# Kernel optimization log

Measured on AMD Instinct MI355X. Metric: run time of the kernel, lower is better.

## Reference

```python
import jax, jax.numpy as jnp
import numpy as np

EPS = 1e-8
TOPK = 12  # hard-coded fallback size in SSP_func


def _cosine(a, b):
    # torch F.cosine_similarity(dim=1): dot / (max(||a||,eps) * max(||b||,eps))
    dot = (a * b).sum(axis=1)
    na = jnp.sqrt((a * a).sum(axis=1))
    nb = jnp.sqrt((b * b).sum(axis=1))
    return dot / (jnp.maximum(na, EPS) * jnp.maximum(nb, EPS))


def _proto(feat, pred_c, thres):
    # feat: (B, C, HW); pred_c: (B, HW) probabilities for one class
    B, C, HW = feat.shape
    mask = pred_c > thres                                   # (B, HW)
    cnt = mask.sum(axis=-1)                                 # (B,)
    masked_mean = (feat * mask[:, None, :].astype(feat.dtype)).sum(-1) / \
        jnp.maximum(cnt, 1).astype(feat.dtype)[:, None]      # (B, C)
    # top-k fallback when no element exceeds threshold
    _, idx = jax.lax.top_k(pred_c, TOPK)                    # (B, TOPK)
    idx_b = jnp.broadcast_to(idx[:, None, :], (B, C, TOPK))
    topk_mean = jnp.take_along_axis(feat, idx_b, axis=-1).mean(-1)  # (B, C)
    return jnp.where((cnt > 0)[:, None], masked_mean, topk_mean)


def _minmax(x):
    return (x - x.min()) / (x.max() - x.min())


def enhence_forward(supp_fp, supp_bp, query_fea, tau):
    B, C, H, W = query_fea.shape
    # similarity_func on support prototypes
    sim_fg = _cosine(query_fea, supp_fp)                    # (B, H, W)
    sim_bg = _cosine(query_fea, supp_bp)
    query_out = jnp.stack([sim_bg, sim_fg], axis=1) * 10.0  # (B, 2, H, W)
    # SSP_func: per-sample threshold mask + topk fallback -> prototypes
    pred = jax.nn.softmax(query_out, axis=1).reshape(B, 2, H * W)
    fg_thres = jax.nn.sigmoid(tau)
    feat = query_fea.reshape(B, C, H * W)
    query_fp = _proto(feat, pred[:, 1], fg_thres)[:, :, None, None]       # (B,C,1,1)
    query_bp = _proto(feat, pred[:, 0], 1.0 - fg_thres)[:, :, None, None]
    # activation maps, global min-max normalized, blend
    act = _minmax(_cosine(query_fea, query_fp)[:, None])    # (B,1,H,W)
    deact = _minmax(_cosine(query_fea, query_bp)[:, None])
    out = query_fea * act + query_fea * (1.0 - deact)
    return out, query_fp, query_bp


def setup_inputs() -> dict:
    key = jax.random.key(0)
    k1, k2, k3 = jax.random.split(key, 3)
    B, C, H, W = 16, 512, 64, 64
    return {
        "supp_fp": jax.random.normal(k1, (B, C, 1, 1), dtype=jnp.float32),
        "supp_bp": jax.random.normal(k2, (B, C, 1, 1), dtype=jnp.float32),
        "query_fea": jax.random.normal(k3, (B, C, H, W), dtype=jnp.float32),
        "tau": jnp.float32(0.5),  # nn.Parameter init value in torch
    }


def reference(supp_fp, supp_bp, query_fea, tau):
    return enhence_forward(supp_fp, supp_bp, query_fea, tau)
```

## Files before the change

### kernel.cpp

```cpp
#include <hip/hip_runtime.h>
#include <math.h>

#define BB 16
#define CC 512
#define HWS 4096
#define EPSV 1e-8f
#define TK 12
#define NEGINF (-3.402823466e+38f)
#define CSPLIT 8
#define CCH (CC / CSPLIT)

typedef float f32x4 __attribute__((ext_vector_type(4)));

#define OFF_PFG 0
#define OFF_PBG (BB * HWS)
#define OFF_QN  (2 * BB * HWS)
#define OFF_CF  (3 * BB * HWS)
#define OFF_CB  (4 * BB * HWS)
#define OFF_SN  (5 * BB * HWS)
#define OFF_PN  (OFF_SN + 2 * BB)
#define OFF_CNT (OFF_PN + 2 * BB)
#define OFF_TKI (OFF_CNT + 2 * BB)
#define OFF_FMMU (OFF_TKI + 2 * BB * TK)
#define OFF_MFG (OFF_FMMU + 16)
#define OFF_MBG (OFF_MFG + BB * 128)
#define OFF_PD1 (OFF_MBG + BB * 128)
#define OFF_PD2 (OFF_PD1 + CSPLIT * BB * HWS)
#define OFF_PQQ (OFF_PD2 + CSPLIT * BB * HWS)

__device__ __forceinline__ float sigmoidf_(float x) { return 1.f / (1.f + expf(-x)); }

__device__ __forceinline__ unsigned encf_(float f) {
    unsigned u = __float_as_uint(f);
    return (u >> 31) ? ~u : (u | 0x80000000u);
}
__device__ __forceinline__ float decf_(unsigned e) {
    return __uint_as_float((e >> 31) ? (e ^ 0x80000000u) : ~e);
}

__global__ void k0_init(const float* __restrict__ sfp, const float* __restrict__ sbp,
                        float* __restrict__ snorm, int* __restrict__ cnts,
                        unsigned* __restrict__ fmmu) {
    if (blockIdx.x == BB) {
        int t = threadIdx.x;
        if (t < 2 * BB) cnts[t] = 0;
        if (t < 4) fmmu[t] = (t & 1) ? 0u : 0xFFFFFFFFu;
        return;
    }
    int b = blockIdx.x;
    int t = threadIdx.x;
    float s1 = 0.f, s2 = 0.f;
    for (int c = t; c < CC; c += 64) {
        float v = sfp[b * CC + c]; s1 += v * v;
        float w = sbp[b * CC + c]; s2 += w * w;
    }
    for (int off = 32; off; off >>= 1) {
        s1 += __shfl_down(s1, off);
        s2 += __shfl_down(s2, off);
    }
    if (t == 0) { snorm[b] = sqrtf(s1); snorm[BB + b] = sqrtf(s2); }
}

__global__ __launch_bounds__(256) void k1_dots(const float* __restrict__ q, const float* __restrict__ sfp,
                        const float* __restrict__ sbp,
                        float* __restrict__ p_df, float* __restrict__ p_db,
                        float* __restrict__ p_qq) {
    int b = blockIdx.z, cs = blockIdx.y;
    int hw4 = blockIdx.x * 256 + threadIdx.x;
    __shared__ float sf[CCH], sb[CCH];
    if (threadIdx.x < CCH) sf[threadIdx.x] = sfp[b * CC + cs * CCH + threadIdx.x];
    else if (threadIdx.x < 2 * CCH) sb[threadIdx.x - CCH] = sbp[b * CC + cs * CCH + (threadIdx.x - CCH)];
    __syncthreads();
    const f32x4* qp4 = (const f32x4*)(q + (size_t)b * CC * HWS + (size_t)cs * CCH * HWS) + hw4;
    f32x4 df = {0, 0, 0, 0}, db = {0, 0, 0, 0}, qq = {0, 0, 0, 0};
#pragma unroll 1
    for (int jj = 0; jj < CCH; jj += 16) {
        f32x4 v[16];
#pragma unroll
        for (int k = 0; k < 16; k++) v[k] = qp4[(size_t)(jj + k) * (HWS / 4)];
#pragma unroll
        for (int k = 0; k < 16; k++) {
            float a = sf[jj + k], c = sb[jj + k];
            df += v[k] * a;
            db += v[k] * c;
            qq += v[k] * v[k];
        }
    }
    size_t o = (size_t)(cs * BB + b) * (HWS / 4) + hw4;
    ((f32x4*)p_df)[o] = df;
    ((f32x4*)p_db)[o] = db;
    ((f32x4*)p_qq)[o] = qq;
}

__global__ __launch_bounds__(256) void k1b_comb(const float* __restrict__ p_df, const float* __restrict__ p_db,
                         const float* __restrict__ p_qq, const float* __restrict__ snorm,
                         const float* __restrict__ tau,
                         float* __restrict__ pfg, float* __restrict__ pbg,
                         float* __restrict__ qn, int* __restrict__ cnts,
                         unsigned* __restrict__ mfg, unsigned* __restrict__ mbg) {
    int b = blockIdx.y;
    int tid = threadIdx.x;
    int hw4 = blockIdx.x * 256 + tid;
    float4 df = {0, 0, 0, 0}, db = {0, 0, 0, 0}, qq = {0, 0, 0, 0};
    for (int cs = 0; cs < CSPLIT; cs++) {
        size_t o = (size_t)(cs * BB + b) * (HWS / 4) + hw4;
        float4 a = ((const float4*)p_df)[o];
        float4 c = ((const float4*)p_db)[o];
        float4 e = ((const float4*)p_qq)[o];
        df.x += a.x; df.y += a.y; df.z += a.z; df.w += a.w;
        db.x += c.x; db.y += c.y; db.z += c.z; db.w += c.w;
        qq.x += e.x; qq.y += e.y; qq.z += e.z; qq.w += e.w;
    }
    float snf = fmaxf(snorm[b], EPSV), snb = fmaxf(snorm[BB + b], EPSV);
    float thres_fg = sigmoidf_(tau[0]);
    float thres_bg = 1.f - thres_fg;
    float dfa[4] = {df.x, df.y, df.z, df.w};
    float dba[4] = {db.x, db.y, db.z, db.w};
    float qqa[4] = {qq.x, qq.y, qq.z, qq.w};
    float pfa[4], pba[4], qna[4];
    unsigned nf = 0, nb = 0;
#pragma unroll
    for (int i = 0; i < 4; i++) {
        float na = sqrtf(qqa[i]);
        float den = fmaxf(na, EPSV);
        float simf = dfa[i] / (den * snf);
        float simb = dba[i] / (den * snb);
        float a = 10.f * simb, c2 = 10.f * simf;
        float m = fmaxf(a, c2);
        float ea = expf(a - m), eb = expf(c2 - m);
        float inv = 1.f / (ea + eb);
        pfa[i] = eb * inv;
        pba[i] = ea * inv;
        qna[i] = na;
        nf |= (pfa[i] > thres_fg ? 1u : 0u) << i;
        nb |= (pba[i] > thres_bg ? 1u : 0u) << i;
    }
    float4 opf = {pfa[0], pfa[1], pfa[2], pfa[3]};
    float4 opb = {pba[0], pba[1], pba[2], pba[3]};
    float4 oqn = {qna[0], qna[1], qna[2], qna[3]};
    size_t o = (size_t)b * (HWS / 4) + hw4;
    ((float4*)pfg)[o] = opf;
    ((float4*)pbg)[o] = opb;
    ((float4*)qn)[o] = oqn;
    __shared__ unsigned char nibf[256], nibb[256];
    nibf[tid] = (unsigned char)nf;
    nibb[tid] = (unsigned char)nb;
    int cfg = __popc(nf), cbg = __popc(nb);
    for (int off = 32; off; off >>= 1) {
        cfg += __shfl_down(cfg, off);
        cbg += __shfl_down(cbg, off);
    }
    if ((tid & 63) == 0) {
        atomicAdd(&cnts[b], cfg);
        atomicAdd(&cnts[BB + b], cbg);
    }
    __syncthreads();
    if (tid < 32) {
        unsigned wf = 0, wb = 0;
#pragma unroll
        for (int k = 0; k < 8; k++) {
            wf |= ((unsigned)nibf[tid * 8 + k]) << (4 * k);
            wb |= ((unsigned)nibb[tid * 8 + k]) << (4 * k);
        }
        mfg[b * 128 + blockIdx.x * 32 + tid] = wf;
        mbg[b * 128 + blockIdx.x * 32 + tid] = wb;
    }
}

__global__ void k2_topk(const float* __restrict__ pfg, const float* __restrict__ pbg,
                        const int* __restrict__ cnts, int* __restrict__ tki) {
    int id = blockIdx.x;
    int cls = id >> 4, b = id & 15;
    if (cnts[cls * BB + b] > 0) return;
    int t = threadIdx.x;
    __shared__ float vals[HWS];
    __shared__ float rv[256];
    __shared__ int   ri[256];
    const float* pr = cls ? pbg : pfg;
    for (int i = t; i < HWS; i += 256) vals[i] = pr[b * HWS + i];
    __syncthreads();
    for (int k = 0; k < TK; k++) {
        float bv = NEGINF; int bi = HWS;
        for (int i = t; i < HWS; i += 256) {
            float v = vals[i];
            if (v > bv) { bv = v; bi = i; }
        }
        rv[t] = bv; ri[t] = bi;
        __syncthreads();
        for (int s = 128; s; s >>= 1) {
            if (t < s) {
                float ov = rv[t + s]; int oi = ri[t + s];
                if (ov > rv[t] || (ov == rv[t] && oi < ri[t])) { rv[t] = ov; ri[t] = oi; }
            }
            __syncthreads();
        }
        if (t == 0) {
            tki[(cls * BB + b) * TK + k] = ri[0];
            vals[ri[0]] = NEGINF;
        }
        __syncthreads();
    }
}

__global__ __launch_bounds__(256) void k3_proto(const float* __restrict__ q,
                         const unsigned* __restrict__ mfg, const unsigned* __restrict__ mbg,
                         const int* __restrict__ cnts, const int* __restrict__ tki,
                         float* __restrict__ out_fp, float* __restrict__ out_bp) {
    int b = blockIdx.y;
    int t = threadIdx.x;
    __shared__ unsigned smf[128], smb[128];
    if (t < 128) smf[t] = mfg[b * 128 + t];
    else smb[t - 128] = mbg[b * 128 + (t - 128)];
    __syncthreads();
    int wave = t >> 6, lane = t & 63;
    int c = blockIdx.x * 4 + wave;
    const float* qp = q + (size_t)b * CC * HWS + (size_t)c * HWS;
    const f32x4* qp4 = (const f32x4*)qp;
    f32x4 v[16];
#pragma unroll
    for (int j = 0; j < 16; j++) v[j] = qp4[j * 64 + lane];
    unsigned wf[16], wb[16];
#pragma unroll
    for (int j = 0; j < 16; j++) {
        int w = j * 8 + (lane >> 3);
        int sh = (lane & 7) * 4;
        wf[j] = smf[w] >> sh;
        wb[j] = smb[w] >> sh;
    }
    float sfv = 0.f, sbv = 0.f;
#pragma unroll
    for (int j = 0; j < 16; j++) {
        sfv += (wf[j] & 1 ? v[j].x : 0.f) + (wf[j] & 2 ? v[j].y : 0.f)
             + (wf[j] & 4 ? v[j].z : 0.f) + (wf[j] & 8 ? v[j].w : 0.f);
        sbv += (wb[j] & 1 ? v[j].x : 0.f) + (wb[j] & 2 ? v[j].y : 0.f)
             + (wb[j] & 4 ? v[j].z : 0.f) + (wb[j] & 8 ? v[j].w : 0.f);
    }
    for (int off = 32; off; off >>= 1) {
        sfv += __shfl_down(sfv, off);
        sbv += __shfl_down(sbv, off);
    }
    if (lane == 0) {
        int cntf = cnts[b], cntb = cnts[BB + b];
        float fpv, bpv;
        if (cntf > 0) fpv = sfv / (float)cntf;
        else {
            float tf = 0.f;
            for (int j = 0; j < TK; j++) tf += qp[tki[b * TK + j]];
            fpv = tf / (float)TK;
        }
        if (cntb > 0) bpv = sbv / (float)cntb;
        else {
            float tb = 0.f;
            for (int j = 0; j < TK; j++) tb += qp[tki[(BB + b) * TK + j]];
            bpv = tb / (float)TK;
        }
        out_fp[b * CC + c] = fpv;
        out_bp[b * CC + c] = bpv;
    }
}

__global__ void k3b_pnorm(const float* __restrict__ ofp, const float* __restrict__ obp,
                          float* __restrict__ pnorm) {
    int b = blockIdx.x;
    int t = threadIdx.x;
    float s1 = 0.f, s2 = 0.f;
    for (int c = t; c < CC; c += 64) {
        float v = ofp[b * CC + c]; s1 += v * v;
        float w = obp[b * CC + c]; s2 += w * w;
    }
    for (int off = 32; off; off >>= 1) {
        s1 += __shfl_down(s1, off);
        s2 += __shfl_down(s2, off);
    }
    if (t == 0) { pnorm[b] = sqrtf(s1); pnorm[BB + b] = sqrtf(s2); }
}

__global__ __launch_bounds__(256) void k4_dots(const float* __restrict__ q, const float* __restrict__ ofp,
                        const float* __restrict__ obp,
                        float* __restrict__ p_df, float* __restrict__ p_db) {
    int b = blockIdx.z, cs = blockIdx.y;
    int hw4 = blockIdx.x * 256 + threadIdx.x;
    __shared__ float pf[CCH], pb[CCH];
    if (threadIdx.x < CCH) pf[threadIdx.x] = ofp[b * CC + cs * CCH + threadIdx.x];
    else if (threadIdx.x < 2 * CCH) pb[threadIdx.x - CCH] = obp[b * CC + cs * CCH + (threadIdx.x - CCH)];
    __syncthreads();
    const f32x4* qp4 = (const f32x4*)(q + (size_t)b * CC * HWS + (size_t)cs * CCH * HWS) + hw4;
    f32x4 df = {0, 0, 0, 0}, db = {0, 0, 0, 0};
#pragma unroll 1
    for (int jj = 0; jj < CCH; jj += 16) {
        f32x4 v[16];
#pragma unroll
        for (int k = 0; k < 16; k++) v[k] = qp4[(size_t)(jj + k) * (HWS / 4)];
#pragma unroll
        for (int k = 0; k < 16; k++) {
            float a = pf[jj + k], c = pb[jj + k];
            df += v[k] * a;
            db += v[k] * c;
        }
    }
    size_t o = (size_t)(cs * BB + b) * (HWS / 4) + hw4;
    ((f32x4*)p_df)[o] = df;
    ((f32x4*)p_db)[o] = db;
}

__global__ __launch_bounds__(256) void k4b_comb(const float* __restrict__ p_df, const float* __restrict__ p_db,
                         const float* __restrict__ pnorm, const float* __restrict__ qn,
                         float* __restrict__ cf, float* __restrict__ cb,
                         unsigned* __restrict__ fmmu) {
    int b = blockIdx.y;
    int hw4 = blockIdx.x * 256 + threadIdx.x;
    float4 df = {0, 0, 0, 0}, db = {0, 0, 0, 0};
    for (int cs = 0; cs < CSPLIT; cs++) {
        size_t o = (size_t)(cs * BB + b) * (HWS / 4) + hw4;
        float4 a = ((const float4*)p_df)[o];
        float4 c = ((const float4*)p_db)[o];
        df.x += a.x; df.y += a.y; df.z += a.z; df.w += a.w;
        db.x += c.x; db.y += c.y; db.z += c.z; db.w += c.w;
    }
    size_t o = (size_t)b * (HWS / 4) + hw4;
    float4 nv = ((const float4*)qn)[o];
    float pnf = fmaxf(pnorm[b], EPSV), pnb = fmaxf(pnorm[BB + b], EPSV);
    float dfa[4] = {df.x, df.y, df.z, df.w};
    float dba[4] = {db.x, db.y, db.z, db.w};
    float nva[4] = {nv.x, nv.y, nv.z, nv.w};
    float cfa[4], cba[4];
    float mnf = 1e38f, mxf = -1e38f, mnb = 1e38f, mxb = -1e38f;
#pragma unroll
    for (int i = 0; i < 4; i++) {
        float na = fmaxf(nva[i], EPSV);
        cfa[i] = dfa[i] / (na * pnf);
        cba[i] = dba[i] / (na * pnb);
        mnf = fminf(mnf, cfa[i]); mxf = fmaxf(mxf, cfa[i]);
        mnb = fminf(mnb, cba[i]); mxb = fmaxf(mxb, cba[i]);
    }
    float4 ocf = {cfa[0], cfa[1], cfa[2], cfa[3]};
    float4 ocb = {cba[0], cba[1], cba[2], cba[3]};
    ((float4*)cf)[o] = ocf;
    ((float4*)cb)[o] = ocb;
    for (int off = 32; off; off >>= 1) {
        mnf = fminf(mnf, __shfl_down(mnf, off));
        mxf = fmaxf(mxf, __shfl_down(mxf, off));
        mnb = fminf(mnb, __shfl_down(mnb, off));
        mxb = fmaxf(mxb, __shfl_down(mxb, off));
    }
    __shared__ float s4[4][4];
    int wave = threadIdx.x >> 6, lane = threadIdx.x & 63;
    if (lane == 0) { s4[wave][0] = mnf; s4[wave][1] = mxf; s4[wave][2] = mnb; s4[wave][3] = mxb; }
    __syncthreads();
    if (threadIdx.x == 0) {
        float a0 = s4[0][0], a1 = s4[0][1], a2 = s4[0][2], a3 = s4[0][3];
        for (int w = 1; w < 4; w++) {
            a0 = fminf(a0, s4[w][0]);
            a1 = fmaxf(a1, s4[w][1]);
            a2 = fminf(a2, s4[w][2]);
            a3 = fmaxf(a3, s4[w][3]);
        }
        atomicMin(&fmmu[0], encf_(a0));
        atomicMax(&fmmu[1], encf_(a1));
        atomicMin(&fmmu[2], encf_(a2));
        atomicMax(&fmmu[3], encf_(a3));
    }
}

__global__ __launch_bounds__(256) void k6_out(const float* __restrict__ q, const float* __restrict__ cf,
                       const float* __restrict__ cb, const unsigned* __restrict__ fmmu,
                       float* __restrict__ out) {
    size_t idx = (size_t)blockIdx.x * 256 + threadIdx.x;
    float mnf = decf_(fmmu[0]), mxf = decf_(fmmu[1]);
    float mnb = decf_(fmmu[2]), mxb = decf_(fmmu[3]);
    float rf = 1.f / (mxf - mnf), rb = 1.f / (mxb - mnb);
    size_t chan = idx >> 10;
    int h4 = (int)(idx & 1023);
    int b = (int)(chan >> 9);
    f32x4 qv = __builtin_nontemporal_load((const f32x4*)q + idx);
    f32x4 c1 = ((const f32x4*)(cf + (size_t)b * HWS))[h4];
    f32x4 c2 = ((const f32x4*)(cb + (size_t)b * HWS))[h4];
    f32x4 o;
    o.x = qv.x * ((c1.x - mnf) * rf) + qv.x * (1.f - (c2.x - mnb) * rb);
    o.y = qv.y * ((c1.y - mnf) * rf) + qv.y * (1.f - (c2.y - mnb) * rb);
    o.z = qv.z * ((c1.z - mnf) * rf) + qv.z * (1.f - (c2.z - mnb) * rb);
    o.w = qv.w * ((c1.w - mnf) * rf) + qv.w * (1.f - (c2.w - mnb) * rb);
    __builtin_nontemporal_store(o, (f32x4*)out + idx);
}

extern "C" void kernel_launch(void* const* d_in, const int* in_sizes, int n_in,
                              void* d_out, int out_size, void* d_ws, size_t ws_size,
                              hipStream_t stream) {
    const float* sfp = (const float*)d_in[0];
    const float* sbp = (const float*)d_in[1];
    const float* q   = (const float*)d_in[2];
    const float* tau = (const float*)d_in[3];
    float* out = (float*)d_out;
    float* wsf = (float*)d_ws;

    float* pfg = wsf + OFF_PFG;
    float* pbg = wsf + OFF_PBG;
    float* qn  = wsf + OFF_QN;
    float* cf  = wsf + OFF_CF;
    float* cb  = wsf + OFF_CB;
    float* snorm = wsf + OFF_SN;
    float* pnorm = wsf + OFF_PN;
    int*   cnts  = (int*)(wsf + OFF_CNT);
    int*   tki   = (int*)(wsf + OFF_TKI);
    unsigned* fmmu = (unsigned*)(wsf + OFF_FMMU);
    unsigned* mfg  = (unsigned*)(wsf + OFF_MFG);
    unsigned* mbg  = (unsigned*)(wsf + OFF_MBG);
    float* p_df  = wsf + OFF_PD1;
    float* p_db  = wsf + OFF_PD2;
    float* p_qq  = wsf + OFF_PQQ;

    float* out_fp = out + (size_t)BB * CC * HWS;
    float* out_bp = out_fp + BB * CC;

    k0_init<<<BB + 1, 64, 0, stream>>>(sfp, sbp, snorm, cnts, fmmu);
    k1_dots<<<dim3(HWS / 1024, CSPLIT, BB), 256, 0, stream>>>(q, sfp, sbp, p_df, p_db, p_qq);
    k1b_comb<<<dim3(HWS / 1024, BB), 256, 0, stream>>>(p_df, p_db, p_qq, snorm, tau, pfg, pbg, qn, cnts, mfg, mbg);
    k2_topk<<<32, 256, 0, stream>>>(pfg, pbg, cnts, tki);
    k3_proto<<<dim3(CC / 4, BB), 256, 0, stream>>>(q, mfg, mbg, cnts, tki, out_fp, out_bp);
    k3b_pnorm<<<BB, 64, 0, stream>>>(out_fp, out_bp, pnorm);
    k4_dots<<<dim3(HWS / 1024, CSPLIT, BB), 256, 0, stream>>>(q, out_fp, out_bp, p_df, p_db);
    k4b_comb<<<dim3(HWS / 1024, BB), 256, 0, stream>>>(p_df, p_db, pnorm, qn, cf, cb, fmmu);
    k6_out<<<(BB * CC * HWS / 4) / 256, 256, 0, stream>>>(q, cf, cb, fmmu, out);
}
```

Before: 322.2 us.

## Rework channel-dot kernels to wave-level tasks with finer channel split

The two channel-reduction dot kernels are restructured so each wavefront owns a (batch, 16-channel slice, 2048-pixel tile) task. Each thread keeps 8 vector accumulators and reads weights directly instead of staging them in shared memory. The channel split grows from 8 to 32, raising parallelism and loads in flight, at the cost of 4x larger partial-sum buffers for the combine kernels to read back. The combine kernels move to 64-thread blocks, and the final output store switches from nontemporal to a normal store.

After: 354.7 us. 10.1% more time.

```diff
diff --git a/kernel.cpp b/kernel.cpp
--- a/kernel.cpp
+++ b/kernel.cpp
@@ -7,8 +7,11 @@
 #define EPSV 1e-8f
 #define TK 12
 #define NEGINF (-3.402823466e+38f)
-#define CSPLIT 8
-#define CCH (CC / CSPLIT)
+
+#define CS2 32
+#define CCH2 (CC / CS2)
+#define PT 2048
+#define NPT (HWS / PT)
 
 typedef float f32x4 __attribute__((ext_vector_type(4)));
 
@@ -25,8 +28,8 @@
 #define OFF_MFG (OFF_FMMU + 16)
 #define OFF_MBG (OFF_MFG + BB * 128)
 #define OFF_PD1 (OFF_MBG + BB * 128)
-#define OFF_PD2 (OFF_PD1 + CSPLIT * BB * HWS)
-#define OFF_PQQ (OFF_PD2 + CSPLIT * BB * HWS)
+#define OFF_PD2 (OFF_PD1 + CS2 * BB * HWS)
+#define OFF_PQQ (OFF_PD2 + CS2 * BB * HWS)
 
 __device__ __forceinline__ float sigmoidf_(float x) { return 1.f / (1.f + expf(-x)); }
 
@@ -65,66 +68,70 @@
                         const float* __restrict__ sbp,
                         float* __restrict__ p_df, float* __restrict__ p_db,
                         float* __restrict__ p_qq) {
-    int b = blockIdx.z, cs = blockIdx.y;
-    int hw4 = blockIdx.x * 256 + threadIdx.x;
-    __shared__ float sf[CCH], sb[CCH];
-    if (threadIdx.x < CCH) sf[threadIdx.x] = sfp[b * CC + cs * CCH + threadIdx.x];
-    else if (threadIdx.x < 2 * CCH) sb[threadIdx.x - CCH] = sbp[b * CC + cs * CCH + (threadIdx.x - CCH)];
-    __syncthreads();
-    const f32x4* qp4 = (const f32x4*)(q + (size_t)b * CC * HWS + (size_t)cs * CCH * HWS) + hw4;
-    f32x4 df = {0, 0, 0, 0}, db = {0, 0, 0, 0}, qq = {0, 0, 0, 0};
+    int wtask = blockIdx.x * 4 + (threadIdx.x >> 6);
+    int lane = threadIdx.x & 63;
+    int pt = wtask & (NPT - 1);
+    int cs = (wtask >> 1) & (CS2 - 1);
+    int b  = wtask >> 6;
+    const f32x4* base = (const f32x4*)(q + (size_t)b * CC * HWS + (size_t)cs * CCH2 * HWS + (size_t)pt * PT);
+    f32x4 df[8], db[8], qq[8];
+#pragma unroll
+    for (int i = 0; i < 8; i++) { df[i] = (f32x4){0,0,0,0}; db[i] = (f32x4){0,0,0,0}; qq[i] = (f32x4){0,0,0,0}; }
 #pragma unroll 1
-    for (int jj = 0; jj < CCH; jj += 16) {
-        f32x4 v[16];
-#pragma unroll
-        for (int k = 0; k < 16; k++) v[k] = qp4[(size_t)(jj + k) * (HWS / 4)];
-#pragma unroll
-        for (int k = 0; k < 16; k++) {
-            float a = sf[jj + k], c = sb[jj + k];
-            df += v[k] * a;
-            db += v[k] * c;
-            qq += v[k] * v[k];
-        }
-    }
-    size_t o = (size_t)(cs * BB + b) * (HWS / 4) + hw4;
-    ((f32x4*)p_df)[o] = df;
-    ((f32x4*)p_db)[o] = db;
-    ((f32x4*)p_qq)[o] = qq;
-}
-
-__global__ __launch_bounds__(256) void k1b_comb(const float* __restrict__ p_df, const float* __restrict__ p_db,
+    for (int c = 0; c < CCH2; c += 2) {
+        float a0 = sfp[b * CC + cs * CCH2 + c];
+        float b0 = sbp[b * CC + cs * CCH2 + c];
+        float a1 = sfp[b * CC + cs * CCH2 + c + 1];
+        float b1 = sbp[b * CC + cs * CCH2 + c + 1];
+        f32x4 v0[8], v1[8];
+#pragma unroll
+        for (int i = 0; i < 8; i++) v0[i] = base[(size_t)c * (HWS / 4) + i * 64 + lane];
+#pragma unroll
+        for (int i = 0; i < 8; i++) v1[i] = base[(size_t)(c + 1) * (HWS / 4) + i * 64 + lane];
+#pragma unroll
+        for (int i = 0; i < 8; i++) {
+            df[i] += v0[i] * a0; df[i] += v1[i] * a1;
+            db[i] += v0[i] * b0; db[i] += v1[i] * b1;
+            qq[i] += v0[i] * v0[i]; qq[i] += v1[i] * v1[i];
+        }
+    }
+    size_t ob = (size_t)(cs * BB + b) * (HWS / 4) + pt * (PT / 4);
+#pragma unroll
+    for (int i = 0; i < 8; i++) {
+        ((f32x4*)p_df)[ob + i * 64 + lane] = df[i];
+        ((f32x4*)p_db)[ob + i * 64 + lane] = db[i];
+        ((f32x4*)p_qq)[ob + i * 64 + lane] = qq[i];
+    }
+}
+
+__global__ __launch_bounds__(64) void k1b_comb(const float* __restrict__ p_df, const float* __restrict__ p_db,
                          const float* __restrict__ p_qq, const float* __restrict__ snorm,
                          const float* __restrict__ tau,
                          float* __restrict__ pfg, float* __restrict__ pbg,
                          float* __restrict__ qn, int* __restrict__ cnts,
                          unsigned* __restrict__ mfg, unsigned* __restrict__ mbg) {
     int b = blockIdx.y;
-    int tid = threadIdx.x;
-    int hw4 = blockIdx.x * 256 + tid;
-    float4 df = {0, 0, 0, 0}, db = {0, 0, 0, 0}, qq = {0, 0, 0, 0};
-    for (int cs = 0; cs < CSPLIT; cs++) {
+    int t = threadIdx.x;
+    int hw4 = blockIdx.x * 64 + t;
+    f32x4 df = {0,0,0,0}, db = {0,0,0,0}, qq = {0,0,0,0};
+#pragma unroll 4
+    for (int cs = 0; cs < CS2; cs++) {
         size_t o = (size_t)(cs * BB + b) * (HWS / 4) + hw4;
-        float4 a = ((const float4*)p_df)[o];
-        float4 c = ((const float4*)p_db)[o];
-        float4 e = ((const float4*)p_qq)[o];
-        df.x += a.x; df.y += a.y; df.z += a.z; df.w += a.w;
-        db.x += c.x; db.y += c.y; db.z += c.z; db.w += c.w;
-        qq.x += e.x; qq.y += e.y; qq.z += e.z; qq.w += e.w;
+        df += ((const f32x4*)p_df)[o];
+        db += ((const f32x4*)p_db)[o];
+        qq += ((const f32x4*)p_qq)[o];
     }
     float snf = fmaxf(snorm[b], EPSV), snb = fmaxf(snorm[BB + b], EPSV);
     float thres_fg = sigmoidf_(tau[0]);
     float thres_bg = 1.f - thres_fg;
-    float dfa[4] = {df.x, df.y, df.z, df.w};
-    float dba[4] = {db.x, db.y, db.z, db.w};
-    float qqa[4] = {qq.x, qq.y, qq.z, qq.w};
     float pfa[4], pba[4], qna[4];
     unsigned nf = 0, nb = 0;
 #pragma unroll
     for (int i = 0; i < 4; i++) {
-        float na = sqrtf(qqa[i]);
+        float na = sqrtf(qq[i]);
         float den = fmaxf(na, EPSV);
-        float simf = dfa[i] / (den * snf);
-        float simb = dba[i] / (den * snb);
+        float simf = df[i] / (den * snf);
+        float simb = db[i] / (den * snb);
         float a = 10.f * simb, c2 = 10.f * simf;
         float m = fmaxf(a, c2);
         float ea = expf(a - m), eb = expf(c2 - m);
@@ -135,35 +142,35 @@
         nf |= (pfa[i] > thres_fg ? 1u : 0u) << i;
         nb |= (pba[i] > thres_bg ? 1u : 0u) << i;
     }
-    float4 opf = {pfa[0], pfa[1], pfa[2], pfa[3]};
-    float4 opb = {pba[0], pba[1], pba[2], pba[3]};
-    float4 oqn = {qna[0], qna[1], qna[2], qna[3]};
+    f32x4 opf = {pfa[0], pfa[1], pfa[2], pfa[3]};
+    f32x4 opb = {pba[0], pba[1], pba[2], pba[3]};
+    f32x4 oqn = {qna[0], qna[1], qna[2], qna[3]};
     size_t o = (size_t)b * (HWS / 4) + hw4;
-    ((float4*)pfg)[o] = opf;
-    ((float4*)pbg)[o] = opb;
-    ((float4*)qn)[o] = oqn;
-    __shared__ unsigned char nibf[256], nibb[256];
-    nibf[tid] = (unsigned char)nf;
-    nibb[tid] = (unsigned char)nb;
+    ((f32x4*)pfg)[o] = opf;
+    ((f32x4*)pbg)[o] = opb;
+    ((f32x4*)qn)[o] = oqn;
+    __shared__ unsigned char nibf[64], nibb[64];
+    nibf[t] = (unsigned char)nf;
+    nibb[t] = (unsigned char)nb;
     int cfg = __popc(nf), cbg = __popc(nb);
     for (int off = 32; off; off >>= 1) {
         cfg += __shfl_down(cfg, off);
         cbg += __shfl_down(cbg, off);
     }
-    if ((tid & 63) == 0) {
+    if (t == 0) {
         atomicAdd(&cnts[b], cfg);
         atomicAdd(&cnts[BB + b], cbg);
     }
     __syncthreads();
-    if (tid < 32) {
+    if (t < 8) {
         unsigned wf = 0, wb = 0;
 #pragma unroll
         for (int k = 0; k < 8; k++) {
-            wf |= ((unsigned)nibf[tid * 8 + k]) << (4 * k);
-            wb |= ((unsigned)nibb[tid * 8 + k]) << (4 * k);
-        }
-        mfg[b * 128 + blockIdx.x * 32 + tid] = wf;
-        mbg[b * 128 + blockIdx.x * 32 + tid] = wb;
+            wf |= ((unsigned)nibf[t * 8 + k]) << (4 * k);
+            wb |= ((unsigned)nibb[t * 8 + k]) << (4 * k);
+        }
+        mfg[b * 128 + blockIdx.x * 8 + t] = wf;
+        mbg[b * 128 + blockIdx.x * 8 + t] = wb;
     }
 }
 
@@ -278,87 +285,81 @@
 __global__ __launch_bounds__(256) void k4_dots(const float* __restrict__ q, const float* __restrict__ ofp,
                         const float* __restrict__ obp,
                         float* __restrict__ p_df, float* __restrict__ p_db) {
-    int b = blockIdx.z, cs = blockIdx.y;
-    int hw4 = blockIdx.x * 256 + threadIdx.x;
-    __shared__ float pf[CCH], pb[CCH];
-    if (threadIdx.x < CCH) pf[threadIdx.x] = ofp[b * CC + cs * CCH + threadIdx.x];
-    else if (threadIdx.x < 2 * CCH) pb[threadIdx.x - CCH] = obp[b * CC + cs * CCH + (threadIdx.x - CCH)];
-    __syncthreads();
-    const f32x4* qp4 = (const f32x4*)(q + (size_t)b * CC * HWS + (size_t)cs * CCH * HWS) + hw4;
-    f32x4 df = {0, 0, 0, 0}, db = {0, 0, 0, 0};
+    int wtask = blockIdx.x * 4 + (threadIdx.x >> 6);
+    int lane = threadIdx.x & 63;
+    int pt = wtask & (NPT - 1);
+    int cs = (wtask >> 1) & (CS2 - 1);
+    int b  = wtask >> 6;
+    const f32x4* base = (const f32x4*)(q + (size_t)b * CC * HWS + (size_t)cs * CCH2 * HWS + (size_t)pt * PT);
+    f32x4 df[8], db[8];
+#pragma unroll
+    for (int i = 0; i < 8; i++) { df[i] = (f32x4){0,0,0,0}; db[i] = (f32x4){0,0,0,0}; }
 #pragma unroll 1
-    for (int jj = 0; jj < CCH; jj += 16) {
-        f32x4 v[16];
-#pragma unroll
-        for (int k = 0; k < 16; k++) v[k] = qp4[(size_t)(jj + k) * (HWS / 4)];
-#pragma unroll
-        for (int k = 0; k < 16; k++) {
-            float a = pf[jj + k], c = pb[jj + k];
-            df += v[k] * a;
-            db += v[k] * c;
-        }
-    }
-    size_t o = (size_t)(cs * BB + b) * (HWS / 4) + hw4;
-    ((f32x4*)p_df)[o] = df;
-    ((f32x4*)p_db)[o] = db;
-}
-
-__global__ __launch_bounds__(256) void k4b_comb(const float* __restrict__ p_df, const float* __restrict__ p_db,
+    for (int c = 0; c < CCH2; c += 2) {
+        float a0 = ofp[b * CC + cs * CCH2 + c];
+        float b0 = obp[b * CC + cs * CCH2 + c];
+        float a1 = ofp[b * CC + cs * CCH2 + c + 1];
+        float b1 = obp[b * CC + cs * CCH2 + c + 1];
+        f32x4 v0[8], v1[8];
+#pragma unroll
+        for (int i = 0; i < 8; i++) v0[i] = base[(size_t)c * (HWS / 4) + i * 64 + lane];
+#pragma unroll
+        for (int i = 0; i < 8; i++) v1[i] = base[(size_t)(c + 1) * (HWS / 4) + i * 64 + lane];
+#pragma unroll
+        for (int i = 0; i < 8; i++) {
+            df[i] += v0[i] * a0; df[i] += v1[i] * a1;
+            db[i] += v0[i] * b0; db[i] += v1[i] * b1;
+        }
+    }
+    size_t ob = (size_t)(cs * BB + b) * (HWS / 4) + pt * (PT / 4);
+#pragma unroll
+    for (int i = 0; i < 8; i++) {
+        ((f32x4*)p_df)[ob + i * 64 + lane] = df[i];
+        ((f32x4*)p_db)[ob + i * 64 + lane] = db[i];
+    }
+}
+
+__global__ __launch_bounds__(64) void k4b_comb(const float* __restrict__ p_df, const float* __restrict__ p_db,
                          const float* __restrict__ pnorm, const float* __restrict__ qn,
                          float* __restrict__ cf, float* __restrict__ cb,
                          unsigned* __restrict__ fmmu) {
     int b = blockIdx.y;
-    int hw4 = blockIdx.x * 256 + threadIdx.x;
-    float4 df = {0, 0, 0, 0}, db = {0, 0, 0, 0};
-    for (int cs = 0; cs < CSPLIT; cs++) {
+    int t = threadIdx.x;
+    int hw4 = blockIdx.x * 64 + t;
+    f32x4 df = {0,0,0,0}, db = {0,0,0,0};
+#pragma unroll 4
+    for (int cs = 0; cs < CS2; cs++) {
         size_t o = (size_t)(cs * BB + b) * (HWS / 4) + hw4;
-        float4 a = ((const float4*)p_df)[o];
-        float4 c = ((const float4*)p_db)[o];
-        df.x += a.x; df.y += a.y; df.z += a.z; df.w += a.w;
-        db.x += c.x; db.y += c.y; db.z += c.z; db.w += c.w;
+        df += ((const f32x4*)p_df)[o];
+        db += ((const f32x4*)p_db)[o];
     }
     size_t o = (size_t)b * (HWS / 4) + hw4;
-    float4 nv = ((const float4*)qn)[o];
+    f32x4 nv = ((const f32x4*)qn)[o];
     float pnf = fmaxf(pnorm[b], EPSV), pnb = fmaxf(pnorm[BB + b], EPSV);
-    float dfa[4] = {df.x, df.y, df.z, df.w};
-    float dba[4] = {db.x, db.y, db.z, db.w};
-    float nva[4] = {nv.x, nv.y, nv.z, nv.w};
-    float cfa[4], cba[4];
+    f32x4 ocf, ocb;
     float mnf = 1e38f, mxf = -1e38f, mnb = 1e38f, mxb = -1e38f;
 #pragma unroll
     for (int i = 0; i < 4; i++) {
-        float na = fmaxf(nva[i], EPSV);
-        cfa[i] = dfa[i] / (na * pnf);
-        cba[i] = dba[i] / (na * pnb);
-        mnf = fminf(mnf, cfa[i]); mxf = fmaxf(mxf, cfa[i]);
-        mnb = fminf(mnb, cba[i]); mxb = fmaxf(mxb, cba[i]);
-    }
-    float4 ocf = {cfa[0], cfa[1], cfa[2], cfa[3]};
-    float4 ocb = {cba[0], cba[1], cba[2], cba[3]};
-    ((float4*)cf)[o] = ocf;
-    ((float4*)cb)[o] = ocb;
+        float na = fmaxf(nv[i], EPSV);
+        float cfv = df[i] / (na * pnf);
+        float cbv = db[i] / (na * pnb);
+        ocf[i] = cfv; ocb[i] = cbv;
+        mnf = fminf(mnf, cfv); mxf = fmaxf(mxf, cfv);
+        mnb = fminf(mnb, cbv); mxb = fmaxf(mxb, cbv);
+    }
+    ((f32x4*)cf)[o] = ocf;
+    ((f32x4*)cb)[o] = ocb;
     for (int off = 32; off; off >>= 1) {
         mnf = fminf(mnf, __shfl_down(mnf, off));
         mxf = fmaxf(mxf, __shfl_down(mxf, off));
         mnb = fminf(mnb, __shfl_down(mnb, off));
         mxb = fmaxf(mxb, __shfl_down(mxb, off));
     }
-    __shared__ float s4[4][4];
-    int wave = threadIdx.x >> 6, lane = threadIdx.x & 63;
-    if (lane == 0) { s4[wave][0] = mnf; s4[wave][1] = mxf; s4[wave][2] = mnb; s4[wave][3] = mxb; }
-    __syncthreads();
-    if (threadIdx.x == 0) {
-        float a0 = s4[0][0], a1 = s4[0][1], a2 = s4[0][2], a3 = s4[0][3];
-        for (int w = 1; w < 4; w++) {
-            a0 = fminf(a0, s4[w][0]);
-            a1 = fmaxf(a1, s4[w][1]);
-            a2 = fminf(a2, s4[w][2]);
-            a3 = fmaxf(a3, s4[w][3]);
-        }
-        atomicMin(&fmmu[0], encf_(a0));
-        atomicMax(&fmmu[1], encf_(a1));
-        atomicMin(&fmmu[2], encf_(a2));
-        atomicMax(&fmmu[3], encf_(a3));
+    if (t == 0) {
+        atomicMin(&fmmu[0], encf_(mnf));
+        atomicMax(&fmmu[1], encf_(mxf));
+        atomicMin(&fmmu[2], encf_(mnb));
+        atomicMax(&fmmu[3], encf_(mxb));
     }
 }
 
@@ -380,7 +381,7 @@
     o.y = qv.y * ((c1.y - mnf) * rf) + qv.y * (1.f - (c2.y - mnb) * rb);
     o.z = qv.z * ((c1.z - mnf) * rf) + qv.z * (1.f - (c2.z - mnb) * rb);
     o.w = qv.w * ((c1.w - mnf) * rf) + qv.w * (1.f - (c2.w - mnb) * rb);
-    __builtin_nontemporal_store(o, (f32x4*)out + idx);
+    ((f32x4*)out)[idx] = o;
 }
 
 extern "C" void kernel_launch(void* const* d_in, const int* in_sizes, int n_in,
@@ -413,12 +414,12 @@
     float* out_bp = out_fp + BB * CC;
 
     k0_init<<<BB + 1, 64, 0, stream>>>(sfp, sbp, snorm, cnts, fmmu);
-    k1_dots<<<dim3(HWS / 1024, CSPLIT, BB), 256, 0, stream>>>(q, sfp, sbp, p_df, p_db, p_qq);
-    k1b_comb<<<dim3(HWS / 1024, BB), 256, 0, stream>>>(p_df, p_db, p_qq, snorm, tau, pfg, pbg, qn, cnts, mfg, mbg);
+    k1_dots<<<NPT * CS2 * BB / 4, 256, 0, stream>>>(q, sfp, sbp, p_df, p_db, p_qq);
+    k1b_comb<<<dim3(HWS / 4 / 64, BB), 64, 0, stream>>>(p_df, p_db, p_qq, snorm, tau, pfg, pbg, qn, cnts, mfg, mbg);
     k2_topk<<<32, 256, 0, stream>>>(pfg, pbg, cnts, tki);
     k3_proto<<<dim3(CC / 4, BB), 256, 0, stream>>>(q, mfg, mbg, cnts, tki, out_fp, out_bp);
     k3b_pnorm<<<BB, 64, 0, stream>>>(out_fp, out_bp, pnorm);
-    k4_dots<<<dim3(HWS / 1024, CSPLIT, BB), 256, 0, stream>>>(q, out_fp, out_bp, p_df, p_db);
-    k4b_comb<<<dim3(HWS / 1024, BB), 256, 0, stream>>>(p_df, p_db, pnorm, qn, cf, cb, fmmu);
+    k4_dots<<<NPT * CS2 * BB / 4, 256, 0, stream>>>(q, out_fp, out_bp, p_df, p_db);
+    k4b_comb<<<dim3(HWS / 4 / 64, BB), 64, 0, stream>>>(p_df, p_db, pnorm, qn, cf, cb, fmmu);
     k6_out<<<(BB * CC * HWS / 4) / 256, 256, 0, stream>>>(q, cf, cb, fmmu, out);
 }
```

## Fuse channel-split dot kernels with combine passes using LDS-staged full-channel loops

Applied to the files above, without the earlier changes.

Replaces the channel-split dot-product kernels and their separate combine kernels with single kernels. Each block owns 256 pixels of one batch and loops over all 512 channels, staging 64-channel tiles through shared memory with register prefetch of the next tile. This drops the partial-sum buffers and the extra launches. Global atomics for mask counts and min/max are replaced by per-block partial results, reduced in the topk kernel and in a new tiny min/max kernel. The trade-off is only 256 blocks, each using 64KB of shared memory, which lowers occupancy and the number of memory requests in flight during the bandwidth-bound passes over the query tensor.

After: 318.9 us. No clear change (-1.0%).

```diff
diff --git a/kernel.cpp b/kernel.cpp
--- a/kernel.cpp
+++ b/kernel.cpp
@@ -7,8 +7,8 @@
 #define EPSV 1e-8f
 #define TK 12
 #define NEGINF (-3.402823466e+38f)
-#define CSPLIT 8
-#define CCH (CC / CSPLIT)
+#define CHG 64
+#define NG (CC / CHG)
 
 typedef float f32x4 __attribute__((ext_vector_type(4)));
 
@@ -21,32 +21,16 @@
 #define OFF_PN  (OFF_SN + 2 * BB)
 #define OFF_CNT (OFF_PN + 2 * BB)
 #define OFF_TKI (OFF_CNT + 2 * BB)
-#define OFF_FMMU (OFF_TKI + 2 * BB * TK)
-#define OFF_MFG (OFF_FMMU + 16)
+#define OFF_FMM (OFF_TKI + 2 * BB * TK)
+#define OFF_PCNT (OFF_FMM + 4)
+#define OFF_BMM (OFF_PCNT + 2 * BB * 16)
+#define OFF_MFG (OFF_BMM + 256 * 4)
 #define OFF_MBG (OFF_MFG + BB * 128)
-#define OFF_PD1 (OFF_MBG + BB * 128)
-#define OFF_PD2 (OFF_PD1 + CSPLIT * BB * HWS)
-#define OFF_PQQ (OFF_PD2 + CSPLIT * BB * HWS)
 
 __device__ __forceinline__ float sigmoidf_(float x) { return 1.f / (1.f + expf(-x)); }
 
-__device__ __forceinline__ unsigned encf_(float f) {
-    unsigned u = __float_as_uint(f);
-    return (u >> 31) ? ~u : (u | 0x80000000u);
-}
-__device__ __forceinline__ float decf_(unsigned e) {
-    return __uint_as_float((e >> 31) ? (e ^ 0x80000000u) : ~e);
-}
-
-__global__ void k0_init(const float* __restrict__ sfp, const float* __restrict__ sbp,
-                        float* __restrict__ snorm, int* __restrict__ cnts,
-                        unsigned* __restrict__ fmmu) {
-    if (blockIdx.x == BB) {
-        int t = threadIdx.x;
-        if (t < 2 * BB) cnts[t] = 0;
-        if (t < 4) fmmu[t] = (t & 1) ? 0u : 0xFFFFFFFFu;
-        return;
-    }
+__global__ void k0_snorm(const float* __restrict__ sfp, const float* __restrict__ sbp,
+                         float* __restrict__ snorm) {
     int b = blockIdx.x;
     int t = threadIdx.x;
     float s1 = 0.f, s2 = 0.f;
@@ -61,118 +45,97 @@
     if (t == 0) { snorm[b] = sqrtf(s1); snorm[BB + b] = sqrtf(s2); }
 }
 
-__global__ __launch_bounds__(256) void k1_dots(const float* __restrict__ q, const float* __restrict__ sfp,
-                        const float* __restrict__ sbp,
-                        float* __restrict__ p_df, float* __restrict__ p_db,
-                        float* __restrict__ p_qq) {
-    int b = blockIdx.z, cs = blockIdx.y;
-    int hw4 = blockIdx.x * 256 + threadIdx.x;
-    __shared__ float sf[CCH], sb[CCH];
-    if (threadIdx.x < CCH) sf[threadIdx.x] = sfp[b * CC + cs * CCH + threadIdx.x];
-    else if (threadIdx.x < 2 * CCH) sb[threadIdx.x - CCH] = sbp[b * CC + cs * CCH + (threadIdx.x - CCH)];
-    __syncthreads();
-    const f32x4* qp4 = (const f32x4*)(q + (size_t)b * CC * HWS + (size_t)cs * CCH * HWS) + hw4;
-    f32x4 df = {0, 0, 0, 0}, db = {0, 0, 0, 0}, qq = {0, 0, 0, 0};
+__device__ __forceinline__ void loadg_(const float* __restrict__ qb, int g, int wid, int lane,
+                                       f32x4* vv) {
+#pragma unroll
+    for (int i = 0; i < 16; i++)
+        vv[i] = *(const f32x4*)(qb + (size_t)(g * CHG + wid + 4 * i) * HWS + lane * 4);
+}
+__device__ __forceinline__ void storel_(float* __restrict__ tile, int wid, int lane,
+                                        const f32x4* vv) {
+#pragma unroll
+    for (int i = 0; i < 16; i++)
+        *(f32x4*)&tile[(wid + 4 * i) * 256 + lane * 4] = vv[i];
+}
+
+__global__ __launch_bounds__(256) void k1f(const float* __restrict__ q,
+        const float* __restrict__ sfp, const float* __restrict__ sbp,
+        const float* __restrict__ snorm, const float* __restrict__ tau,
+        float* __restrict__ pfg, float* __restrict__ pbg, float* __restrict__ qn,
+        int* __restrict__ pcnt, unsigned* __restrict__ mfg, unsigned* __restrict__ mbg) {
+    int chunk = blockIdx.x, b = blockIdx.y;
+    int tid = threadIdx.x, lane = tid & 63, wid = tid >> 6;
+    __shared__ float tile[CHG * 256];
+    __shared__ int wcf[4], wcb[4];
+    const float* qb = q + (size_t)b * CC * HWS + (size_t)chunk * 256;
+    const float* sfb = sfp + b * CC;
+    const float* sbb = sbp + b * CC;
+    float df = 0.f, db = 0.f, qq = 0.f;
+    f32x4 v[16];
+    loadg_(qb, 0, wid, lane, v);
 #pragma unroll 1
-    for (int jj = 0; jj < CCH; jj += 16) {
-        f32x4 v[16];
-#pragma unroll
-        for (int k = 0; k < 16; k++) v[k] = qp4[(size_t)(jj + k) * (HWS / 4)];
-#pragma unroll
-        for (int k = 0; k < 16; k++) {
-            float a = sf[jj + k], c = sb[jj + k];
-            df += v[k] * a;
-            db += v[k] * c;
-            qq += v[k] * v[k];
-        }
-    }
-    size_t o = (size_t)(cs * BB + b) * (HWS / 4) + hw4;
-    ((f32x4*)p_df)[o] = df;
-    ((f32x4*)p_db)[o] = db;
-    ((f32x4*)p_qq)[o] = qq;
-}
-
-__global__ __launch_bounds__(256) void k1b_comb(const float* __restrict__ p_df, const float* __restrict__ p_db,
-                         const float* __restrict__ p_qq, const float* __restrict__ snorm,
-                         const float* __restrict__ tau,
-                         float* __restrict__ pfg, float* __restrict__ pbg,
-                         float* __restrict__ qn, int* __restrict__ cnts,
-                         unsigned* __restrict__ mfg, unsigned* __restrict__ mbg) {
-    int b = blockIdx.y;
-    int tid = threadIdx.x;
-    int hw4 = blockIdx.x * 256 + tid;
-    float4 df = {0, 0, 0, 0}, db = {0, 0, 0, 0}, qq = {0, 0, 0, 0};
-    for (int cs = 0; cs < CSPLIT; cs++) {
-        size_t o = (size_t)(cs * BB + b) * (HWS / 4) + hw4;
-        float4 a = ((const float4*)p_df)[o];
-        float4 c = ((const float4*)p_db)[o];
-        float4 e = ((const float4*)p_qq)[o];
-        df.x += a.x; df.y += a.y; df.z += a.z; df.w += a.w;
-        db.x += c.x; db.y += c.y; db.z += c.z; db.w += c.w;
-        qq.x += e.x; qq.y += e.y; qq.z += e.z; qq.w += e.w;
-    }
-    float snf = fmaxf(snorm[b], EPSV), snb = fmaxf(snorm[BB + b], EPSV);
+    for (int g = 0; g < NG; g++) {
+        if (g) __syncthreads();
+        storel_(tile, wid, lane, v);
+        __syncthreads();
+        if (g + 1 < NG) loadg_(qb, g + 1, wid, lane, v);
+#pragma unroll
+        for (int c = 0; c < CHG; c++) {
+            float vv = tile[c * 256 + tid];
+            df = fmaf(vv, sfb[g * CHG + c], df);
+            db = fmaf(vv, sbb[g * CHG + c], db);
+            qq = fmaf(vv, vv, qq);
+        }
+    }
     float thres_fg = sigmoidf_(tau[0]);
     float thres_bg = 1.f - thres_fg;
-    float dfa[4] = {df.x, df.y, df.z, df.w};
-    float dba[4] = {db.x, db.y, db.z, db.w};
-    float qqa[4] = {qq.x, qq.y, qq.z, qq.w};
-    float pfa[4], pba[4], qna[4];
-    unsigned nf = 0, nb = 0;
-#pragma unroll
-    for (int i = 0; i < 4; i++) {
-        float na = sqrtf(qqa[i]);
-        float den = fmaxf(na, EPSV);
-        float simf = dfa[i] / (den * snf);
-        float simb = dba[i] / (den * snb);
-        float a = 10.f * simb, c2 = 10.f * simf;
-        float m = fmaxf(a, c2);
-        float ea = expf(a - m), eb = expf(c2 - m);
-        float inv = 1.f / (ea + eb);
-        pfa[i] = eb * inv;
-        pba[i] = ea * inv;
-        qna[i] = na;
-        nf |= (pfa[i] > thres_fg ? 1u : 0u) << i;
-        nb |= (pba[i] > thres_bg ? 1u : 0u) << i;
-    }
-    float4 opf = {pfa[0], pfa[1], pfa[2], pfa[3]};
-    float4 opb = {pba[0], pba[1], pba[2], pba[3]};
-    float4 oqn = {qna[0], qna[1], qna[2], qna[3]};
-    size_t o = (size_t)b * (HWS / 4) + hw4;
-    ((float4*)pfg)[o] = opf;
-    ((float4*)pbg)[o] = opb;
-    ((float4*)qn)[o] = oqn;
-    __shared__ unsigned char nibf[256], nibb[256];
-    nibf[tid] = (unsigned char)nf;
-    nibb[tid] = (unsigned char)nb;
-    int cfg = __popc(nf), cbg = __popc(nb);
-    for (int off = 32; off; off >>= 1) {
-        cfg += __shfl_down(cfg, off);
-        cbg += __shfl_down(cbg, off);
-    }
-    if ((tid & 63) == 0) {
-        atomicAdd(&cnts[b], cfg);
-        atomicAdd(&cnts[BB + b], cbg);
-    }
-    __syncthreads();
-    if (tid < 32) {
-        unsigned wf = 0, wb = 0;
-#pragma unroll
-        for (int k = 0; k < 8; k++) {
-            wf |= ((unsigned)nibf[tid * 8 + k]) << (4 * k);
-            wb |= ((unsigned)nibb[tid * 8 + k]) << (4 * k);
-        }
-        mfg[b * 128 + blockIdx.x * 32 + tid] = wf;
-        mbg[b * 128 + blockIdx.x * 32 + tid] = wb;
+    float snf = fmaxf(snorm[b], EPSV), snb = fmaxf(snorm[BB + b], EPSV);
+    float na = sqrtf(qq);
+    float den = fmaxf(na, EPSV);
+    float simf = df / (den * snf);
+    float simb = db / (den * snb);
+    float a = 10.f * simb, c2 = 10.f * simf;
+    float m = fmaxf(a, c2);
+    float ea = expf(a - m), eb = expf(c2 - m);
+    float inv = 1.f / (ea + eb);
+    float pf = eb * inv, pb = ea * inv;
+    int p = chunk * 256 + tid;
+    pfg[b * HWS + p] = pf;
+    pbg[b * HWS + p] = pb;
+    qn[b * HWS + p] = na;
+    unsigned long long balf = __ballot(pf > thres_fg);
+    unsigned long long balb = __ballot(pb > thres_bg);
+    if (lane == 0) {
+        mfg[b * 128 + (p >> 5)] = (unsigned)balf;
+        mbg[b * 128 + (p >> 5)] = (unsigned)balb;
+        wcf[wid] = (int)__popcll(balf);
+        wcb[wid] = (int)__popcll(balb);
+    } else if (lane == 32) {
+        mfg[b * 128 + (p >> 5)] = (unsigned)(balf >> 32);
+        mbg[b * 128 + (p >> 5)] = (unsigned)(balb >> 32);
+    }
+    __syncthreads();
+    if (tid == 0) {
+        pcnt[(0 * BB + b) * 16 + chunk] = wcf[0] + wcf[1] + wcf[2] + wcf[3];
+        pcnt[(1 * BB + b) * 16 + chunk] = wcb[0] + wcb[1] + wcb[2] + wcb[3];
     }
 }
 
 __global__ void k2_topk(const float* __restrict__ pfg, const float* __restrict__ pbg,
-                        const int* __restrict__ cnts, int* __restrict__ tki) {
+                        const int* __restrict__ pcnt, int* __restrict__ cnts,
+                        int* __restrict__ tki) {
     int id = blockIdx.x;
     int cls = id >> 4, b = id & 15;
-    if (cnts[cls * BB + b] > 0) return;
-    int t = threadIdx.x;
+    int t = threadIdx.x;
+    __shared__ int cnt_s;
+    if (t == 0) {
+        int s = 0;
+        for (int j = 0; j < 16; j++) s += pcnt[(cls * BB + b) * 16 + j];
+        cnts[cls * BB + b] = s;
+        cnt_s = s;
+    }
+    __syncthreads();
+    if (cnt_s > 0) return;
     __shared__ float vals[HWS];
     __shared__ float rv[256];
     __shared__ int   ri[256];
@@ -275,79 +238,50 @@
     if (t == 0) { pnorm[b] = sqrtf(s1); pnorm[BB + b] = sqrtf(s2); }
 }
 
-__global__ __launch_bounds__(256) void k4_dots(const float* __restrict__ q, const float* __restrict__ ofp,
-                        const float* __restrict__ obp,
-                        float* __restrict__ p_df, float* __restrict__ p_db) {
-    int b = blockIdx.z, cs = blockIdx.y;
-    int hw4 = blockIdx.x * 256 + threadIdx.x;
-    __shared__ float pf[CCH], pb[CCH];
-    if (threadIdx.x < CCH) pf[threadIdx.x] = ofp[b * CC + cs * CCH + threadIdx.x];
-    else if (threadIdx.x < 2 * CCH) pb[threadIdx.x - CCH] = obp[b * CC + cs * CCH + (threadIdx.x - CCH)];
-    __syncthreads();
-    const f32x4* qp4 = (const f32x4*)(q + (size_t)b * CC * HWS + (size_t)cs * CCH * HWS) + hw4;
-    f32x4 df = {0, 0, 0, 0}, db = {0, 0, 0, 0};
+__global__ __launch_bounds__(256) void k4f(const float* __restrict__ q,
+        const float* __restrict__ ofp, const float* __restrict__ obp,
+        const float* __restrict__ pnorm, const float* __restrict__ qn,
+        float* __restrict__ cf, float* __restrict__ cb, float* __restrict__ bmm) {
+    int chunk = blockIdx.x, b = blockIdx.y;
+    int tid = threadIdx.x, lane = tid & 63, wid = tid >> 6;
+    __shared__ float tile[CHG * 256];
+    __shared__ float s4[4][4];
+    const float* qb = q + (size_t)b * CC * HWS + (size_t)chunk * 256;
+    const float* pfb = ofp + b * CC;
+    const float* pbb = obp + b * CC;
+    float df = 0.f, db = 0.f;
+    f32x4 v[16];
+    loadg_(qb, 0, wid, lane, v);
 #pragma unroll 1
-    for (int jj = 0; jj < CCH; jj += 16) {
-        f32x4 v[16];
-#pragma unroll
-        for (int k = 0; k < 16; k++) v[k] = qp4[(size_t)(jj + k) * (HWS / 4)];
-#pragma unroll
-        for (int k = 0; k < 16; k++) {
-            float a = pf[jj + k], c = pb[jj + k];
-            df += v[k] * a;
-            db += v[k] * c;
-        }
-    }
-    size_t o = (size_t)(cs * BB + b) * (HWS / 4) + hw4;
-    ((f32x4*)p_df)[o] = df;
-    ((f32x4*)p_db)[o] = db;
-}
-
-__global__ __launch_bounds__(256) void k4b_comb(const float* __restrict__ p_df, const float* __restrict__ p_db,
-                         const float* __restrict__ pnorm, const float* __restrict__ qn,
-                         float* __restrict__ cf, float* __restrict__ cb,
-                         unsigned* __restrict__ fmmu) {
-    int b = blockIdx.y;
-    int hw4 = blockIdx.x * 256 + threadIdx.x;
-    float4 df = {0, 0, 0, 0}, db = {0, 0, 0, 0};
-    for (int cs = 0; cs < CSPLIT; cs++) {
-        size_t o = (size_t)(cs * BB + b) * (HWS / 4) + hw4;
-        float4 a = ((const float4*)p_df)[o];
-        float4 c = ((const float4*)p_db)[o];
-        df.x += a.x; df.y += a.y; df.z += a.z; df.w += a.w;
-        db.x += c.x; db.y += c.y; db.z += c.z; db.w += c.w;
-    }
-    size_t o = (size_t)b * (HWS / 4) + hw4;
-    float4 nv = ((const float4*)qn)[o];
+    for (int g = 0; g < NG; g++) {
+        if (g) __syncthreads();
+        storel_(tile, wid, lane, v);
+        __syncthreads();
+        if (g + 1 < NG) loadg_(qb, g + 1, wid, lane, v);
+#pragma unroll
+        for (int c = 0; c < CHG; c++) {
+            float vv = tile[c * 256 + tid];
+            df = fmaf(vv, pfb[g * CHG + c], df);
+            db = fmaf(vv, pbb[g * CHG + c], db);
+        }
+    }
     float pnf = fmaxf(pnorm[b], EPSV), pnb = fmaxf(pnorm[BB + b], EPSV);
-    float dfa[4] = {df.x, df.y, df.z, df.w};
-    float dba[4] = {db.x, db.y, db.z, db.w};
-    float nva[4] = {nv.x, nv.y, nv.z, nv.w};
-    float cfa[4], cba[4];
-    float mnf = 1e38f, mxf = -1e38f, mnb = 1e38f, mxb = -1e38f;
-#pragma unroll
-    for (int i = 0; i < 4; i++) {
-        float na = fmaxf(nva[i], EPSV);
-        cfa[i] = dfa[i] / (na * pnf);
-        cba[i] = dba[i] / (na * pnb);
-        mnf = fminf(mnf, cfa[i]); mxf = fmaxf(mxf, cfa[i]);
-        mnb = fminf(mnb, cba[i]); mxb = fmaxf(mxb, cba[i]);
-    }
-    float4 ocf = {cfa[0], cfa[1], cfa[2], cfa[3]};
-    float4 ocb = {cba[0], cba[1], cba[2], cba[3]};
-    ((float4*)cf)[o] = ocf;
-    ((float4*)cb)[o] = ocb;
+    int p = chunk * 256 + tid;
+    float na = fmaxf(qn[b * HWS + p], EPSV);
+    float cfv = df / (na * pnf);
+    float cbv = db / (na * pnb);
+    cf[b * HWS + p] = cfv;
+    cb[b * HWS + p] = cbv;
+    float mnf = cfv, mxf = cfv, mnb2 = cbv, mxb2 = cbv;
     for (int off = 32; off; off >>= 1) {
         mnf = fminf(mnf, __shfl_down(mnf, off));
         mxf = fmaxf(mxf, __shfl_down(mxf, off));
-        mnb = fminf(mnb, __shfl_down(mnb, off));
-        mxb = fmaxf(mxb, __shfl_down(mxb, off));
-    }
-    __shared__ float s4[4][4];
-    int wave = threadIdx.x >> 6, lane = threadIdx.x & 63;
-    if (lane == 0) { s4[wave][0] = mnf; s4[wave][1] = mxf; s4[wave][2] = mnb; s4[wave][3] = mxb; }
-    __syncthreads();
-    if (threadIdx.x == 0) {
+        mnb2 = fminf(mnb2, __shfl_down(mnb2, off));
+        mxb2 = fmaxf(mxb2, __shfl_down(mxb2, off));
+    }
+    if (lane == 0) { s4[wid][0] = mnf; s4[wid][1] = mxf; s4[wid][2] = mnb2; s4[wid][3] = mxb2; }
+    __syncthreads();
+    if (tid == 0) {
         float a0 = s4[0][0], a1 = s4[0][1], a2 = s4[0][2], a3 = s4[0][3];
         for (int w = 1; w < 4; w++) {
             a0 = fminf(a0, s4[w][0]);
@@ -355,20 +289,42 @@
             a2 = fminf(a2, s4[w][2]);
             a3 = fmaxf(a3, s4[w][3]);
         }
-        atomicMin(&fmmu[0], encf_(a0));
-        atomicMax(&fmmu[1], encf_(a1));
-        atomicMin(&fmmu[2], encf_(a2));
-        atomicMax(&fmmu[3], encf_(a3));
+        int bid = b * 16 + chunk;
+        bmm[bid * 4 + 0] = a0;
+        bmm[bid * 4 + 1] = a1;
+        bmm[bid * 4 + 2] = a2;
+        bmm[bid * 4 + 3] = a3;
+    }
+}
+
+__global__ void k5_minmax(const float* __restrict__ bmm, float* __restrict__ fmm) {
+    int t = threadIdx.x;
+    float mnf = 1e38f, mxf = -1e38f, mnb = 1e38f, mxb = -1e38f;
+    for (int j = t; j < 256; j += 64) {
+        mnf = fminf(mnf, bmm[j * 4 + 0]);
+        mxf = fmaxf(mxf, bmm[j * 4 + 1]);
+        mnb = fminf(mnb, bmm[j * 4 + 2]);
+        mxb = fmaxf(mxb, bmm[j * 4 + 3]);
+    }
+    for (int off = 32; off; off >>= 1) {
+        mnf = fminf(mnf, __shfl_down(mnf, off));
+        mxf = fmaxf(mxf, __shfl_down(mxf, off));
+        mnb = fminf(mnb, __shfl_down(mnb, off));
+        mxb = fmaxf(mxb, __shfl_down(mxb, off));
+    }
+    if (t == 0) {
+        fmm[0] = mnf;
+        fmm[1] = 1.f / (mxf - mnf);
+        fmm[2] = mnb;
+        fmm[3] = 1.f / (mxb - mnb);
     }
 }
 
 __global__ __launch_bounds__(256) void k6_out(const float* __restrict__ q, const float* __restrict__ cf,
-                       const float* __restrict__ cb, const unsigned* __restrict__ fmmu,
+                       const float* __restrict__ cb, const float* __restrict__ fmm,
                        float* __restrict__ out) {
     size_t idx = (size_t)blockIdx.x * 256 + threadIdx.x;
-    float mnf = decf_(fmmu[0]), mxf = decf_(fmmu[1]);
-    float mnb = decf_(fmmu[2]), mxb = decf_(fmmu[3]);
-    float rf = 1.f / (mxf - mnf), rb = 1.f / (mxb - mnb);
+    float mnf = fmm[0], rf = fmm[1], mnb = fmm[2], rb = fmm[3];
     size_t chan = idx >> 10;
     int h4 = (int)(idx & 1023);
     int b = (int)(chan >> 9);
@@ -402,23 +358,21 @@
     float* pnorm = wsf + OFF_PN;
     int*   cnts  = (int*)(wsf + OFF_CNT);
     int*   tki   = (int*)(wsf + OFF_TKI);
-    unsigned* fmmu = (unsigned*)(wsf + OFF_FMMU);
-    unsigned* mfg  = (unsigned*)(wsf + OFF_MFG);
-    unsigned* mbg  = (unsigned*)(wsf + OFF_MBG);
-    float* p_df  = wsf + OFF_PD1;
-    float* p_db  = wsf + OFF_PD2;
-    float* p_qq  = wsf + OFF_PQQ;
+    float* fmm   = wsf + OFF_FMM;
+    int*   pcnt  = (int*)(wsf + OFF_PCNT);
+    float* bmm   = wsf + OFF_BMM;
+    unsigned* mfg = (unsigned*)(wsf + OFF_MFG);
+    unsigned* mbg = (unsigned*)(wsf + OFF_MBG);
 
     float* out_fp = out + (size_t)BB * CC * HWS;
     float* out_bp = out_fp + BB * CC;
 
-    k0_init<<<BB + 1, 64, 0, stream>>>(sfp, sbp, snorm, cnts, fmmu);
-    k1_dots<<<dim3(HWS / 1024, CSPLIT, BB), 256, 0, stream>>>(q, sfp, sbp, p_df, p_db, p_qq);
-    k1b_comb<<<dim3(HWS / 1024, BB), 256, 0, stream>>>(p_df, p_db, p_qq, snorm, tau, pfg, pbg, qn, cnts, mfg, mbg);
-    k2_topk<<<32, 256, 0, stream>>>(pfg, pbg, cnts, tki);
+    k0_snorm<<<BB, 64, 0, stream>>>(sfp, sbp, snorm);
+    k1f<<<dim3(16, BB), 256, 0, stream>>>(q, sfp, sbp, snorm, tau, pfg, pbg, qn, pcnt, mfg, mbg);
+    k2_topk<<<32, 256, 0, stream>>>(pfg, pbg, pcnt, cnts, tki);
     k3_proto<<<dim3(CC / 4, BB), 256, 0, stream>>>(q, mfg, mbg, cnts, tki, out_fp, out_bp);
     k3b_pnorm<<<BB, 64, 0, stream>>>(out_fp, out_bp, pnorm);
-    k4_dots<<<dim3(HWS / 1024, CSPLIT, BB), 256, 0, stream>>>(q, out_fp, out_bp, p_df, p_db);
-    k4b_comb<<<dim3(HWS / 1024, BB), 256, 0, stream>>>(p_df, p_db, pnorm, qn, cf, cb, fmmu);
-    k6_out<<<(BB * CC * HWS / 4) / 256, 256, 0, stream>>>(q, cf, cb, fmmu, out);
-}
+    k4f<<<dim3(16, BB), 256, 0, stream>>>(q, out_fp, out_bp, pnorm, qn, cf, cb, bmm);
+    k5_minmax<<<1, 64, 0, stream>>>(bmm, fmm);
+    k6_out<<<(BB * CC * HWS / 4) / 256, 256, 0, stream>>>(q, cf, cb, fmm, out);
+}
```
